# Kernel tuning notes

Hardware: AMD Instinct MI355X
Metric: run time of the kernel (lower is better)

Reference implementation:

```python
import jax, jax.numpy as jnp
import numpy as np

N = 8192
NHID = 256

def setup_inputs() -> dict:
    key = jax.random.key(0)
    ks = jax.random.split(key, 9)
    s = 1.0 / np.sqrt(NHID)  # torch Linear default init scale
    return {
        "x1": jax.random.normal(ks[0], (N, NHID), jnp.float32),
        "x2": jax.random.normal(ks[1], (N, NHID), jnp.float32),
        "x3": jax.random.normal(ks[2], (N, NHID), jnp.float32),
        "Wq": jax.random.uniform(ks[3], (NHID, NHID), jnp.float32, -s, s),
        "bq": jax.random.uniform(ks[4], (NHID,), jnp.float32, -s, s),
        "Wk": jax.random.uniform(ks[5], (NHID, NHID), jnp.float32, -s, s),
        "bk": jax.random.uniform(ks[6], (NHID,), jnp.float32, -s, s),
        "Wv": jax.random.uniform(ks[7], (NHID, NHID), jnp.float32, -s, s),
        "bv": jax.random.uniform(ks[8], (NHID,), jnp.float32, -s, s),
    }

def reference(x1, x2, x3, Wq, bq, Wk, bk, Wv, bv):
    # torch.nn.Linear: y = x @ W.T + b
    q = x1 @ Wq.T + bq                      # [N, nhid]
    k = x2 @ Wk.T + bk                      # [N, nhid]
    v = x3 @ Wv.T + bv                      # [N, nhid]
    scores = q @ k.T                        # [N, N], NOTE: unscaled (no 1/sqrt(d))
    attn = jax.nn.softmax(scores, axis=1)   # softmax over keys (dim=1)
    return attn @ v                         # [N, nhid]
```

## Files before the change

kernel.cpp:

```cpp
#include <hip/hip_runtime.h>
#include <stdint.h>

typedef unsigned short u16;
typedef __attribute__((ext_vector_type(8))) short short8;
typedef __attribute__((ext_vector_type(4))) float f32x4;

#define LOG2E 1.4426950408889634f
#define NT 8192
#define DH 256

#define QH     0
#define KH     2097152
#define VTB    4194304
#define OPARTB 6291456
#define XH0 6291456
#define XL0 8388608
#define XH1 10485760
#define XL1 12582912
#define XH2 14680064
#define XL2 16777216
#define WQH 18874368
#define WQL 18939904
#define WKH 19005440
#define WKL 19070976
#define WVH 19136512
#define WVL 19202048
#define MPART_F 11534336
#define LPART_F 11599872

__device__ __forceinline__ u16 f2bf(float f) {
  union { float f; uint32_t u; } c; c.f = f;
  uint32_t u = c.u;
  return (u16)((u + 0x7fffu + ((u >> 16) & 1)) >> 16);
}
__device__ __forceinline__ u16 f2bf_hu(float f) {
  union { float f; uint32_t u; } c; c.f = f;
  return (u16)((c.u + 0x8000u) >> 16);
}
__device__ __forceinline__ float bf2f(u16 h) {
  union { uint32_t u; float f; } c; c.u = ((uint32_t)h) << 16;
  return c.f;
}

__device__ __forceinline__ int swz32(int u, int h) {
  return (u & 24) | ((u & 7) ^ (h & 7));
}

__device__ __forceinline__ f32x4 mfma16(short8 a, short8 b, f32x4 c) {
  return __builtin_amdgcn_mfma_f32_16x16x32_bf16(a, b, c, 0, 0, 0);
}

__device__ __forceinline__ void gl_lds16(const u16* g, u16* l) {
  __builtin_amdgcn_global_load_lds(
      (const __attribute__((address_space(1))) uint32_t*)g,
      (__attribute__((address_space(3))) uint32_t*)l, 16, 0, 0);
}

__global__ __launch_bounds__(256) void k_convert(
    const float* __restrict__ x1, const float* __restrict__ x2, const float* __restrict__ x3,
    const float* __restrict__ wq, const float* __restrict__ wk, const float* __restrict__ wv,
    u16* __restrict__ wsu) {
  int b = blockIdx.x;
  const float* src; u16 *dh, *dl; int bl;
  if (b < 1024)      { src = x1; dh = wsu + XH0; dl = wsu + XL0; bl = b; }
  else if (b < 2048) { src = x2; dh = wsu + XH1; dl = wsu + XL1; bl = b - 1024; }
  else if (b < 3072) { src = x3; dh = wsu + XH2; dl = wsu + XL2; bl = b - 2048; }
  else if (b < 3104) { src = wq; dh = wsu + WQH; dl = wsu + WQL; bl = b - 3072; }
  else if (b < 3136) { src = wk; dh = wsu + WKH; dl = wsu + WKL; bl = b - 3104; }
  else               { src = wv; dh = wsu + WVH; dl = wsu + WVL; bl = b - 3136; }
  int i = (bl * 256 + threadIdx.x) * 8;
  f32x4 a = *(const f32x4*)(src + i);
  f32x4 c = *(const f32x4*)(src + i + 4);
  short8 rh, rl;
  float v[8] = {a[0], a[1], a[2], a[3], c[0], c[1], c[2], c[3]};
#pragma unroll
  for (int j = 0; j < 8; j++) {
    u16 h = f2bf(v[j]);
    rh[j] = (short)h;
    rl[j] = (short)f2bf(v[j] - bf2f(h));
  }
  *(short8*)(dh + i) = rh;
  *(short8*)(dl + i) = rl;
}

__global__ __launch_bounds__(256) void k_qkv(
    u16* __restrict__ wsu,
    const float* __restrict__ bq, const float* __restrict__ bk, const float* __restrict__ bv) {
  __shared__ u16 sAh[32 * 256];
  __shared__ u16 sAl[32 * 256];
  __shared__ u16 sBh[32 * 256];
  __shared__ u16 sBl[32 * 256];
  int bx = blockIdx.x;
  int mid = bx >> 8;
  int t = bx & 255;
  const u16 *Ah, *Al, *Bh, *Bl; u16 *O; const float* bias;
  int rowA0, colBase, ldO, biasRow;
  if (mid == 0) {
    Ah = wsu + XH0; Al = wsu + XL0; Bh = wsu + WQH; Bl = wsu + WQL;
    O = wsu + QH; bias = bq; biasRow = 0; ldO = 256;
    rowA0 = t * 32; colBase = 0;
  } else if (mid == 1) {
    Ah = wsu + XH1; Al = wsu + XL1; Bh = wsu + WKH; Bl = wsu + WKL;
    O = wsu + KH; bias = bk; biasRow = 0; ldO = 256;
    rowA0 = t * 32; colBase = 0;
  } else {
    Ah = wsu + WVH; Al = wsu + WVL; Bh = wsu + XH2; Bl = wsu + XL2;
    O = wsu + VTB; bias = bv; biasRow = 1; ldO = 8192;
    rowA0 = (t & 7) * 32; colBase = (t >> 3) * 256;
  }

  int tid = threadIdx.x;
  int lane = tid & 63, wave = tid >> 6;
  int n = lane & 15, quad = lane >> 4;
  int wm = wave >> 1, wn = wave & 1;

#pragma unroll
  for (int i = 0; i < 4; i++) {
    int L = i * 256 + tid;
    int row = L >> 5, u = L & 31;
    short8 vh = *(const short8*)(Ah + (size_t)(rowA0 + row) * 256 + u * 8);
    short8 vl = *(const short8*)(Al + (size_t)(rowA0 + row) * 256 + u * 8);
    *(short8*)(&sAh[row * 256 + swz32(u, row) * 8]) = vh;
    *(short8*)(&sAl[row * 256 + swz32(u, row) * 8]) = vl;
  }

  int brow0 = wave * 2 + (lane >> 5);
  int bgu = (lane & 24) | ((lane & 7) ^ (brow0 & 7));

#pragma unroll
  for (int i = 0; i < 4; i++) {
    gl_lds16(Bh + (size_t)(colBase + i * 8 + brow0) * 256 + bgu * 8, &sBh[i * 2048 + wave * 512]);
    gl_lds16(Bl + (size_t)(colBase + i * 8 + brow0) * 256 + bgu * 8, &sBl[i * 2048 + wave * 512]);
  }

#pragma unroll 1
  for (int g = 0; g < 8; g++) {
    __syncthreads();

    int colg = colBase + g * 32 + wn * 16 + n;
    f32x4 acc = {0.f, 0.f, 0.f, 0.f};
#pragma unroll
    for (int kk = 0; kk < 8; kk++) {
      int ra = wm * 16 + n;
      int rbB = wn * 16 + n;
      short8 ah = *(const short8*)(&sAh[ra * 256 + swz32(kk * 4 + quad, ra) * 8]);
      short8 al = *(const short8*)(&sAl[ra * 256 + swz32(kk * 4 + quad, ra) * 8]);
      short8 bh = *(const short8*)(&sBh[rbB * 256 + swz32(kk * 4 + quad, rbB) * 8]);
      short8 bl = *(const short8*)(&sBl[rbB * 256 + swz32(kk * 4 + quad, rbB) * 8]);
      acc = mfma16(ah, bh, acc);
      acc = mfma16(ah, bl, acc);
      acc = mfma16(al, bh, acc);
    }

    if (g < 7) {
      __syncthreads();
      int b0 = colBase + (g + 1) * 32;
#pragma unroll
      for (int i = 0; i < 4; i++) {
        gl_lds16(Bh + (size_t)(b0 + i * 8 + brow0) * 256 + bgu * 8, &sBh[i * 2048 + wave * 512]);
        gl_lds16(Bl + (size_t)(b0 + i * 8 + brow0) * 256 + bgu * 8, &sBl[i * 2048 + wave * 512]);
      }
    }

    float bcol = biasRow ? 0.0f : bias[colg];
#pragma unroll
    for (int r = 0; r < 4; r++) {
      int rowg = rowA0 + wm * 16 + quad * 4 + r;
      float bb = biasRow ? bias[rowg] : bcol;
      O[(size_t)rowg * ldO + colg] = f2bf(acc[r] + bb);
    }
  }
}

__global__ __launch_bounds__(256, 2) void k_flash(
    const u16* __restrict__ wsu, u16* __restrict__ opart, float* __restrict__ wsf) {
  __shared__ u16 sK[2][32 * 256];
  __shared__ u16 sV[2][256 * 32];
  __shared__ u16 sP[4 * 32 * 40];

  int qb = blockIdx.x >> 3, sp = blockIdx.x & 7;
  int tid = threadIdx.x, lane = tid & 63, wave = tid >> 6;
  int n = lane & 15, quad = lane >> 4;
  const u16* Qp = wsu + QH;
  const u16* Kp = wsu + KH;
  const u16* Vp = wsu + VTB;

  short8 qf[2][8];
  int rowQ0 = qb * 128 + wave * 32 + n;
#pragma unroll
  for (int mt = 0; mt < 2; mt++)
#pragma unroll
    for (int kk = 0; kk < 8; kk++)
      qf[mt][kk] = *(const short8*)(Qp + (size_t)(rowQ0 + mt * 16) * 256 + kk * 32 + quad * 8);

  int krow0 = wave * 2 + (lane >> 5);
  int kh0 = (krow0 >> 1) & 7;
  int kgu0 = (lane & 24) | ((lane & 7) ^ kh0);
  int kgu1 = kgu0 ^ 4;
  int vd_base = wave * 16 + (lane >> 2);
  int vgu = (lane & 3) ^ ((lane >> 3) & 3);

  int key00 = sp * 1024;

#pragma unroll
  for (int i = 0; i < 4; i++) {
    int ku = (i & 1) ? kgu1 : kgu0;
    gl_lds16(Kp + (size_t)(key00 + i * 8 + krow0) * 256 + ku * 8,
             &sK[0][i * 2048 + wave * 512]);
    gl_lds16(Vp + (size_t)(i * 64 + vd_base) * 8192 + key00 + vgu * 8,
             &sV[0][i * 2048 + wave * 512]);
  }

  f32x4 o[2][16];
#pragma unroll
  for (int mt = 0; mt < 2; mt++)
#pragma unroll
    for (int nt = 0; nt < 16; nt++) { o[mt][nt][0]=0.f; o[mt][nt][1]=0.f; o[mt][nt][2]=0.f; o[mt][nt][3]=0.f; }
  float negm0L[8], lcur[8];
#pragma unroll
  for (int j = 0; j < 8; j++) { negm0L[j] = 0.f; lcur[j] = 0.f; }

  for (int it = 0; it < 32; it++) {
    __syncthreads();
    int cur = it & 1;
    if (it + 1 < 32) {
      int k1 = key00 + (it + 1) * 32;
#pragma unroll
      for (int i = 0; i < 4; i++) {
        int ku = (i & 1) ? kgu1 : kgu0;
        gl_lds16(Kp + (size_t)(k1 + i * 8 + krow0) * 256 + ku * 8,
                 &sK[cur ^ 1][i * 2048 + wave * 512]);
        gl_lds16(Vp + (size_t)(i * 64 + vd_base) * 8192 + k1 + vgu * 8,
                 &sV[cur ^ 1][i * 2048 + wave * 512]);
      }
    }

    f32x4 s00={0.f,0.f,0.f,0.f}, s01={0.f,0.f,0.f,0.f};
    f32x4 s10={0.f,0.f,0.f,0.f}, s11={0.f,0.f,0.f,0.f};
#pragma unroll
    for (int kk = 0; kk < 8; kk++) {
      int su = swz32(kk * 4 + quad, n) * 8;
      short8 b0 = *(const short8*)(&sK[cur][(2 * n) * 256 + su]);
      short8 b1 = *(const short8*)(&sK[cur][(2 * n) * 256 + 256 + su]);
      s00 = mfma16(qf[0][kk], b0, s00);
      s01 = mfma16(qf[0][kk], b1, s01);
      s10 = mfma16(qf[1][kk], b0, s10);
      s11 = mfma16(qf[1][kk], b1, s11);
    }

    if (it == 0) {
#pragma unroll
      for (int mt = 0; mt < 2; mt++)
#pragma unroll
        for (int r = 0; r < 4; r++) {
          float v = mt ? fmaxf(s10[r], s11[r]) : fmaxf(s00[r], s01[r]);
          v = fmaxf(v, __shfl_xor(v, 1));
          v = fmaxf(v, __shfl_xor(v, 2));
          v = fmaxf(v, __shfl_xor(v, 4));
          v = fmaxf(v, __shfl_xor(v, 8));
          negm0L[mt * 4 + r] = -v * LOG2E;
        }
    }

    u16* myP = &sP[wave * 1280];
#pragma unroll
    for (int mt = 0; mt < 2; mt++)
#pragma unroll
      for (int r = 0; r < 4; r++) {
        int j = mt * 4 + r;
        float sv0 = mt ? s10[r] : s00[r];
        float sv1 = mt ? s11[r] : s01[r];
        float x0 = fminf(fmaf(sv0, LOG2E, negm0L[j]), 110.f);
        float x1 = fminf(fmaf(sv1, LOG2E, negm0L[j]), 110.f);
        float p0 = exp2f(x0);
        float p1 = exp2f(x1);
        lcur[j] += p0 + p1;
        int row = mt * 16 + quad * 4 + r;
        uint32_t pk = (uint32_t)f2bf_hu(p0) | ((uint32_t)f2bf_hu(p1) << 16);
        *(uint32_t*)&myP[row * 40 + 2 * n] = pk;
      }

    short8 pa0 = *(const short8*)(&myP[n * 40 + quad * 8]);
    short8 pa1 = *(const short8*)(&myP[(16 + n) * 40 + quad * 8]);
#pragma unroll
    for (int nt = 0; nt < 16; nt++) {
      int d = nt * 16 + n;
      short8 vb = *(const short8*)(&sV[cur][d * 32 + (quad ^ ((n >> 1) & 3)) * 8]);
      o[0][nt] = mfma16(pa0, vb, o[0][nt]);
      o[1][nt] = mfma16(pa1, vb, o[1][nt]);
    }
  }

#pragma unroll
  for (int j = 0; j < 8; j++) {
    float v = lcur[j];
    v += __shfl_xor(v, 1); v += __shfl_xor(v, 2);
    v += __shfl_xor(v, 4); v += __shfl_xor(v, 8);
    lcur[j] = v;
  }

  u16* op = opart + (size_t)sp * (NT * DH);
  int rowb = qb * 128 + wave * 32;
#pragma unroll
  for (int mt = 0; mt < 2; mt++)
#pragma unroll
    for (int nt = 0; nt < 16; nt++)
#pragma unroll
      for (int r = 0; r < 4; r++) {
        int row = rowb + mt * 16 + quad * 4 + r;
        op[(size_t)row * 256 + nt * 16 + n] = f2bf(o[mt][nt][r]);
      }
  if (n == 0) {
#pragma unroll
    for (int j = 0; j < 8; j++) {
      int row = rowb + (j >> 2) * 16 + quad * 4 + (j & 3);
      wsf[MPART_F + sp * NT + row] = negm0L[j] * -0.6931471805599453f;
      wsf[LPART_F + sp * NT + row] = lcur[j];
    }
  }
}

__global__ __launch_bounds__(256) void k_combine(
    const u16* __restrict__ opart, const float* __restrict__ wsf, float* __restrict__ out) {
  int gid = blockIdx.x * 256 + threadIdx.x;
  int row = gid >> 6, cg = gid & 63;
  float m[8], l[8];
#pragma unroll
  for (int s = 0; s < 8; s++) {
    m[s] = wsf[MPART_F + s * NT + row];
    l[s] = wsf[LPART_F + s * NT + row];
  }
  float ms = m[0];
#pragma unroll
  for (int s = 1; s < 8; s++) ms = fmaxf(ms, m[s]);
  float denom = 0.f;
  float acc[4] = {0.f, 0.f, 0.f, 0.f};
#pragma unroll
  for (int s = 0; s < 8; s++) {
    float w = exp2f((m[s] - ms) * LOG2E);
    denom += w * l[s];
    const u16* pp = opart + ((size_t)s * NT + row) * 256 + cg * 4;
    uint2 v = *(const uint2*)pp;
    acc[0] += w * bf2f((u16)(v.x & 0xffff));
    acc[1] += w * bf2f((u16)(v.x >> 16));
    acc[2] += w * bf2f((u16)(v.y & 0xffff));
    acc[3] += w * bf2f((u16)(v.y >> 16));
  }
  float inv = 1.0f / denom;
  f32x4 r = {acc[0] * inv, acc[1] * inv, acc[2] * inv, acc[3] * inv};
  *(f32x4*)(out + (size_t)row * 256 + cg * 4) = r;
}

extern "C" void kernel_launch(void* const* d_in, const int* in_sizes, int n_in,
                              void* d_out, int out_size, void* d_ws, size_t ws_size,
                              hipStream_t stream) {
  const float* x1 = (const float*)d_in[0];
  const float* x2 = (const float*)d_in[1];
  const float* x3 = (const float*)d_in[2];
  const float* Wq = (const float*)d_in[3];
  const float* bq = (const float*)d_in[4];
  const float* Wk = (const float*)d_in[5];
  const float* bk = (const float*)d_in[6];
  const float* Wv = (const float*)d_in[7];
  const float* bv = (const float*)d_in[8];
  u16* wsu = (u16*)d_ws;
  float* wsf = (float*)d_ws;
  float* out = (float*)d_out;

  k_convert<<<dim3(3168), dim3(256), 0, stream>>>(x1, x2, x3, Wq, Wk, Wv, wsu);
  k_qkv<<<dim3(768), dim3(256), 0, stream>>>(wsu, bq, bk, bv);
  k_flash<<<dim3(512), dim3(256), 0, stream>>>(wsu, wsu + OPARTB, wsf);
  k_combine<<<dim3(2048), dim3(256), 0, stream>>>(wsu + OPARTB, wsf, out);
}
```

Baseline: 220.4 us.

## Rewrite flash kernel with 32x32 MFMA, transposed S, and register-resident P

Rewrites the split-K flash attention kernel to use 32x32x16 bf16 MFMA, computing S transposed (K as the A operand) so each lane owns one query row. The P tile is packed with v_cvt_pk_bf16_f32 and permlane32_swap and kept in registers, removing the LDS round trip for P. The cross-lane max and sum reductions shrink to a single shuffle. Output is staged through swizzled LDS for 16-byte coalesced stores, and s_setprio is raised around the MFMA loops. The cost is heavier register pressure from 8 f32x16 accumulators plus 16 Q fragments, and new swizzle layouts that must stay correct.

```diff
diff --git a/kernel.cpp b/kernel.cpp
--- a/kernel.cpp
+++ b/kernel.cpp
@@ -4,6 +4,7 @@
 typedef unsigned short u16;
 typedef __attribute__((ext_vector_type(8))) short short8;
 typedef __attribute__((ext_vector_type(4))) float f32x4;
+typedef __attribute__((ext_vector_type(16))) float f32x16;
 
 #define LOG2E 1.4426950408889634f
 #define NT 8192
@@ -33,10 +34,6 @@
   uint32_t u = c.u;
   return (u16)((u + 0x7fffu + ((u >> 16) & 1)) >> 16);
 }
-__device__ __forceinline__ u16 f2bf_hu(float f) {
-  union { float f; uint32_t u; } c; c.f = f;
-  return (u16)((c.u + 0x8000u) >> 16);
-}
 __device__ __forceinline__ float bf2f(u16 h) {
   union { uint32_t u; float f; } c; c.u = ((uint32_t)h) << 16;
   return c.f;
@@ -48,6 +45,9 @@
 
 __device__ __forceinline__ f32x4 mfma16(short8 a, short8 b, f32x4 c) {
   return __builtin_amdgcn_mfma_f32_16x16x32_bf16(a, b, c, 0, 0, 0);
+}
+__device__ __forceinline__ f32x16 mfma32(short8 a, short8 b, f32x16 c) {
+  return __builtin_amdgcn_mfma_f32_32x32x16_bf16(a, b, c, 0, 0, 0);
 }
 
 __device__ __forceinline__ void gl_lds16(const u16* g, u16* l) {
@@ -174,149 +174,153 @@
 
 __global__ __launch_bounds__(256, 2) void k_flash(
     const u16* __restrict__ wsu, u16* __restrict__ opart, float* __restrict__ wsf) {
-  __shared__ u16 sK[2][32 * 256];
-  __shared__ u16 sV[2][256 * 32];
-  __shared__ u16 sP[4 * 32 * 40];
+  __shared__ u16 smem[32768];
 
   int qb = blockIdx.x >> 3, sp = blockIdx.x & 7;
   int tid = threadIdx.x, lane = tid & 63, wave = tid >> 6;
-  int n = lane & 15, quad = lane >> 4;
+  int key = lane & 31;
+  int h = lane >> 5;
   const u16* Qp = wsu + QH;
   const u16* Kp = wsu + KH;
   const u16* Vp = wsu + VTB;
 
-  short8 qf[2][8];
-  int rowQ0 = qb * 128 + wave * 32 + n;
-#pragma unroll
-  for (int mt = 0; mt < 2; mt++)
-#pragma unroll
-    for (int kk = 0; kk < 8; kk++)
-      qf[mt][kk] = *(const short8*)(Qp + (size_t)(rowQ0 + mt * 16) * 256 + kk * 32 + quad * 8);
-
-  int krow0 = wave * 2 + (lane >> 5);
-  int kh0 = (krow0 >> 1) & 7;
-  int kgu0 = (lane & 24) | ((lane & 7) ^ kh0);
-  int kgu1 = kgu0 ^ 4;
+  int rowQ0 = qb * 128 + wave * 32;
+
+  short8 qf[16];
+#pragma unroll
+  for (int kk = 0; kk < 16; kk++)
+    qf[kk] = *(const short8*)(Qp + (size_t)(rowQ0 + key) * 256 + kk * 16 + h * 8);
+
+  int koff[4];
+#pragma unroll
+  for (int m = 0; m < 4; m++)
+    koff[m] = key * 512 + 16 * ((2 * m + h) ^ (key & 7));
+  int voff[2];
+#pragma unroll
+  for (int c = 0; c < 2; c++)
+    voff[c] = key * 64 + 16 * ((2 * c + h) ^ (key & 3));
+
+  int krow0 = wave * 2 + h;
+  int kgu = (lane & 24) | ((lane & 7) ^ (krow0 & 7));
   int vd_base = wave * 16 + (lane >> 2);
-  int vgu = (lane & 3) ^ ((lane >> 3) & 3);
+  int vgu = (lane & 3) ^ ((lane >> 2) & 3);
 
   int key00 = sp * 1024;
 
 #pragma unroll
   for (int i = 0; i < 4; i++) {
-    int ku = (i & 1) ? kgu1 : kgu0;
-    gl_lds16(Kp + (size_t)(key00 + i * 8 + krow0) * 256 + ku * 8,
-             &sK[0][i * 2048 + wave * 512]);
+    gl_lds16(Kp + (size_t)(key00 + i * 8 + krow0) * 256 + kgu * 8,
+             &smem[i * 2048 + wave * 512]);
     gl_lds16(Vp + (size_t)(i * 64 + vd_base) * 8192 + key00 + vgu * 8,
-             &sV[0][i * 2048 + wave * 512]);
-  }
-
-  f32x4 o[2][16];
-#pragma unroll
-  for (int mt = 0; mt < 2; mt++)
-#pragma unroll
-    for (int nt = 0; nt < 16; nt++) { o[mt][nt][0]=0.f; o[mt][nt][1]=0.f; o[mt][nt][2]=0.f; o[mt][nt][3]=0.f; }
-  float negm0L[8], lcur[8];
-#pragma unroll
-  for (int j = 0; j < 8; j++) { negm0L[j] = 0.f; lcur[j] = 0.f; }
-
+             &smem[16384 + i * 2048 + wave * 512]);
+  }
+
+  f32x16 o[8];
+#pragma unroll
+  for (int dt = 0; dt < 8; dt++)
+#pragma unroll
+    for (int r = 0; r < 16; r++) o[dt][r] = 0.f;
+  float negm0 = 0.f, lcur = 0.f;
+
+#pragma unroll 1
   for (int it = 0; it < 32; it++) {
     __syncthreads();
     int cur = it & 1;
+    const u16* sKc = &smem[cur * 8192];
+    const u16* sVc = &smem[16384 + cur * 8192];
     if (it + 1 < 32) {
       int k1 = key00 + (it + 1) * 32;
+      int nb = cur ^ 1;
 #pragma unroll
       for (int i = 0; i < 4; i++) {
-        int ku = (i & 1) ? kgu1 : kgu0;
-        gl_lds16(Kp + (size_t)(k1 + i * 8 + krow0) * 256 + ku * 8,
-                 &sK[cur ^ 1][i * 2048 + wave * 512]);
+        gl_lds16(Kp + (size_t)(k1 + i * 8 + krow0) * 256 + kgu * 8,
+                 &smem[nb * 8192 + i * 2048 + wave * 512]);
         gl_lds16(Vp + (size_t)(i * 64 + vd_base) * 8192 + k1 + vgu * 8,
-                 &sV[cur ^ 1][i * 2048 + wave * 512]);
+                 &smem[16384 + nb * 8192 + i * 2048 + wave * 512]);
       }
     }
 
-    f32x4 s00={0.f,0.f,0.f,0.f}, s01={0.f,0.f,0.f,0.f};
-    f32x4 s10={0.f,0.f,0.f,0.f}, s11={0.f,0.f,0.f,0.f};
-#pragma unroll
-    for (int kk = 0; kk < 8; kk++) {
-      int su = swz32(kk * 4 + quad, n) * 8;
-      short8 b0 = *(const short8*)(&sK[cur][(2 * n) * 256 + su]);
-      short8 b1 = *(const short8*)(&sK[cur][(2 * n) * 256 + 256 + su]);
-      s00 = mfma16(qf[0][kk], b0, s00);
-      s01 = mfma16(qf[0][kk], b1, s01);
-      s10 = mfma16(qf[1][kk], b0, s10);
-      s11 = mfma16(qf[1][kk], b1, s11);
-    }
+    f32x16 s;
+#pragma unroll
+    for (int r = 0; r < 16; r++) s[r] = 0.f;
+    __builtin_amdgcn_s_setprio(1);
+#pragma unroll
+    for (int kk = 0; kk < 16; kk++) {
+      short8 kf = *(const short8*)((const char*)sKc + koff[kk & 3] + 128 * (kk >> 2));
+      s = mfma32(kf, qf[kk], s);
+    }
+    __builtin_amdgcn_s_setprio(0);
 
     if (it == 0) {
-#pragma unroll
-      for (int mt = 0; mt < 2; mt++)
-#pragma unroll
-        for (int r = 0; r < 4; r++) {
-          float v = mt ? fmaxf(s10[r], s11[r]) : fmaxf(s00[r], s01[r]);
-          v = fmaxf(v, __shfl_xor(v, 1));
-          v = fmaxf(v, __shfl_xor(v, 2));
-          v = fmaxf(v, __shfl_xor(v, 4));
-          v = fmaxf(v, __shfl_xor(v, 8));
-          negm0L[mt * 4 + r] = -v * LOG2E;
-        }
-    }
-
-    u16* myP = &sP[wave * 1280];
-#pragma unroll
-    for (int mt = 0; mt < 2; mt++)
-#pragma unroll
-      for (int r = 0; r < 4; r++) {
-        int j = mt * 4 + r;
-        float sv0 = mt ? s10[r] : s00[r];
-        float sv1 = mt ? s11[r] : s01[r];
-        float x0 = fminf(fmaf(sv0, LOG2E, negm0L[j]), 110.f);
-        float x1 = fminf(fmaf(sv1, LOG2E, negm0L[j]), 110.f);
-        float p0 = exp2f(x0);
-        float p1 = exp2f(x1);
-        lcur[j] += p0 + p1;
-        int row = mt * 16 + quad * 4 + r;
-        uint32_t pk = (uint32_t)f2bf_hu(p0) | ((uint32_t)f2bf_hu(p1) << 16);
-        *(uint32_t*)&myP[row * 40 + 2 * n] = pk;
-      }
-
-    short8 pa0 = *(const short8*)(&myP[n * 40 + quad * 8]);
-    short8 pa1 = *(const short8*)(&myP[(16 + n) * 40 + quad * 8]);
-#pragma unroll
-    for (int nt = 0; nt < 16; nt++) {
-      int d = nt * 16 + n;
-      short8 vb = *(const short8*)(&sV[cur][d * 32 + (quad ^ ((n >> 1) & 3)) * 8]);
-      o[0][nt] = mfma16(pa0, vb, o[0][nt]);
-      o[1][nt] = mfma16(pa1, vb, o[1][nt]);
-    }
-  }
-
-#pragma unroll
-  for (int j = 0; j < 8; j++) {
-    float v = lcur[j];
-    v += __shfl_xor(v, 1); v += __shfl_xor(v, 2);
-    v += __shfl_xor(v, 4); v += __shfl_xor(v, 8);
-    lcur[j] = v;
-  }
-
+      float mv = s[0];
+#pragma unroll
+      for (int r = 1; r < 16; r++) mv = fmaxf(mv, s[r]);
+      mv = fmaxf(mv, __shfl_xor(mv, 32));
+      negm0 = -mv * LOG2E;
+    }
+
+    uint32_t c8[8];
+#pragma unroll
+    for (int j = 0; j < 8; j++) {
+      float x0 = fminf(fmaf(s[2 * j],     LOG2E, negm0), 110.f);
+      float x1 = fminf(fmaf(s[2 * j + 1], LOG2E, negm0), 110.f);
+      float p0 = exp2f(x0);
+      float p1 = exp2f(x1);
+      lcur += p0 + p1;
+      asm("v_cvt_pk_bf16_f32 %0, %1, %2" : "=v"(c8[j]) : "v"(p0), "v"(p1));
+    }
+    uint32_t w0a = c8[0], w2a = c8[2], w1a = c8[1], w3a = c8[3];
+    asm("v_permlane32_swap_b32 %0, %1" : "+v"(w0a), "+v"(w2a));
+    asm("v_permlane32_swap_b32 %0, %1" : "+v"(w1a), "+v"(w3a));
+    uint32_t w0b = c8[4], w2b = c8[6], w1b = c8[5], w3b = c8[7];
+    asm("v_permlane32_swap_b32 %0, %1" : "+v"(w0b), "+v"(w2b));
+    asm("v_permlane32_swap_b32 %0, %1" : "+v"(w1b), "+v"(w3b));
+    union { uint32_t u[4]; short8 s8; } pb0, pb1;
+    pb0.u[0] = w0a; pb0.u[1] = w1a; pb0.u[2] = w2a; pb0.u[3] = w3a;
+    pb1.u[0] = w0b; pb1.u[1] = w1b; pb1.u[2] = w2b; pb1.u[3] = w3b;
+
+    __builtin_amdgcn_s_setprio(1);
+#pragma unroll
+    for (int dt = 0; dt < 8; dt++) {
+      short8 v0 = *(const short8*)((const char*)sVc + voff[0] + dt * 2048);
+      o[dt] = mfma32(v0, pb0.s8, o[dt]);
+    }
+#pragma unroll
+    for (int dt = 0; dt < 8; dt++) {
+      short8 v1 = *(const short8*)((const char*)sVc + voff[1] + dt * 2048);
+      o[dt] = mfma32(v1, pb1.s8, o[dt]);
+    }
+    __builtin_amdgcn_s_setprio(0);
+  }
+
+  lcur += __shfl_xor(lcur, 32);
+
+  __syncthreads();
+  u16* tb = &smem[wave * 8192];
+#pragma unroll
+  for (int dt = 0; dt < 8; dt++)
+#pragma unroll
+    for (int j = 0; j < 4; j++) {
+      uint32_t a, b;
+      asm("v_cvt_pk_bf16_f32 %0, %1, %2" : "=v"(a) : "v"(o[dt][4 * j + 0]), "v"(o[dt][4 * j + 1]));
+      asm("v_cvt_pk_bf16_f32 %0, %1, %2" : "=v"(b) : "v"(o[dt][4 * j + 2]), "v"(o[dt][4 * j + 3]));
+      int u16i = (dt * 4 + j) ^ (key & 7);
+      uint2 val; val.x = a; val.y = b;
+      *(uint2*)((char*)tb + key * 512 + u16i * 16 + h * 8) = val;
+    }
   u16* op = opart + (size_t)sp * (NT * DH);
-  int rowb = qb * 128 + wave * 32;
-#pragma unroll
-  for (int mt = 0; mt < 2; mt++)
-#pragma unroll
-    for (int nt = 0; nt < 16; nt++)
-#pragma unroll
-      for (int r = 0; r < 4; r++) {
-        int row = rowb + mt * 16 + quad * 4 + r;
-        op[(size_t)row * 256 + nt * 16 + n] = f2bf(o[mt][nt][r]);
-      }
-  if (n == 0) {
-#pragma unroll
-    for (int j = 0; j < 8; j++) {
-      int row = rowb + (j >> 2) * 16 + quad * 4 + (j & 3);
-      wsf[MPART_F + sp * NT + row] = negm0L[j] * -0.6931471805599453f;
-      wsf[LPART_F + sp * NT + row] = lcur[j];
-    }
+#pragma unroll
+  for (int c2i = 0; c2i < 16; c2i++) {
+    int rl = c2i * 2 + h;
+    int uu = lane & 31;
+    short8 vv = *(const short8*)((const char*)tb + rl * 512 + ((uu ^ (rl & 7)) * 16));
+    *(short8*)(op + (size_t)(rowQ0 + rl) * 256 + uu * 8) = vv;
+  }
+
+  if (lane < 32) {
+    int row = rowQ0 + key;
+    wsf[MPART_F + sp * NT + row] = negm0 * -0.6931471805599453f;
+    wsf[LPART_F + sp * NT + row] = lcur;
   }
 }
 
```

Measured after the change: 208.0 us. -5.6%, faster.
